# Kernel tuning notes

Measured on AMD Instinct MI355X. Metric: run time of the kernel, lower is better.

Reference implementation:

```python
import jax, jax.numpy as jnp
import numpy as np

TAU = 0.7        # init kwarg tau
BIG_NEG = -1.0e9 # matches torch big_neg
B, R = 8192, 4096


def setup_inputs() -> dict:
    key = jax.random.key(0)
    k1, k2 = jax.random.split(key)
    s = jax.random.normal(k1, (B, R), dtype=jnp.float32)
    mask = jax.random.uniform(k2, (B, R), dtype=jnp.float32)  # compared against 0.5
    return {"s": s, "mask": mask, "k": 8}


def reference(s, mask, k):
    # mask-apply then temperature scale
    z = jnp.where(mask > 0.5, s, jnp.full_like(s, BIG_NEG)) / max(TAU, 1e-6)
    # sparsemax along axis 1: sort descending, cumsum, support-size threshold
    z_sorted = -jnp.sort(-z, axis=1)                       # [B, R] descending
    z_cumsum = jnp.cumsum(z_sorted, axis=1)                # [B, R]
    r = jnp.arange(1, R + 1, dtype=z.dtype)[None, :]       # [1, R] ranks 1..R
    cond = 1.0 + r * z_sorted > z_cumsum                   # [B, R] support indicator
    k_sup = jnp.sum(cond, axis=1, keepdims=True)           # [B, 1] int support size
    tau_star = (jnp.take_along_axis(z_cumsum, k_sup - 1, axis=1) - 1.0) / k_sup.astype(z.dtype)
    p = jnp.maximum(z - tau_star, 0.0)                     # sparsemax probs, sum=1
    # scale by budget k and clip to [0, 1]
    return jnp.minimum(jnp.asarray(float(k), z.dtype) * p, 1.0)
```

## Files before the change

### kernel.cpp

```cpp
#include <hip/hip_runtime.h>


#define R_DIM 4096
#define LANES 64
#define CHUNKS (R_DIM / (LANES * 4))
#define ROWS_PER_BLOCK 4
#define BIG_NEG -1.0e9f
#define INV_TAU (1.0f / 0.7f)

__global__ __launch_bounds__(256, 2)
void gate_sparsemax_k_kernel(const float* __restrict__ s,
                             const float* __restrict__ m,
                             const int*  __restrict__ kptr,
                             float* __restrict__ out,
                             int nrows)
{
    __shared__ float zs[ROWS_PER_BLOCK][R_DIM];

    const int lane = (int)(threadIdx.x & 63u);
    const int wid  = (int)(threadIdx.x >> 6);
    const int row  = blockIdx.x * ROWS_PER_BLOCK + wid;
    if (row >= nrows) return;

    const float kf = (float)(*kptr);

    const size_t base = (size_t)row * R_DIM;
    const float4* sv4 = (const float4*)(s + base);
    const float4* mv4 = (const float4*)(m + base);
    float4*       ov4 = (float4*)(out + base);
    float4*       zr4 = (float4*)(zs[wid]);

    float zmax = -3.4028235e38f;
    #pragma unroll
    for (int c = 0; c < CHUNKS; ++c) {
        const int idx = c * LANES + lane;
        const float4 sv = sv4[idx];
        const float4 mv = mv4[idx];
        float4 zv;
        zv.x = (mv.x > 0.5f ? sv.x : BIG_NEG) * INV_TAU;
        zv.y = (mv.y > 0.5f ? sv.y : BIG_NEG) * INV_TAU;
        zv.z = (mv.z > 0.5f ? sv.z : BIG_NEG) * INV_TAU;
        zv.w = (mv.w > 0.5f ? sv.w : BIG_NEG) * INV_TAU;
        zr4[idx] = zv;
        zmax = fmaxf(zmax, fmaxf(fmaxf(zv.x, zv.y), fmaxf(zv.z, zv.w)));
    }

    #pragma unroll
    for (int off = 32; off >= 1; off >>= 1)
        zmax = fmaxf(zmax, __shfl_xor(zmax, off, 64));

    float tau = zmax - 1.0f;
    for (int it = 0; it < 50; ++it) {
        float ssum = 0.0f;
        float cnt  = 0.0f;
        #pragma unroll
        for (int c = 0; c < CHUNKS; ++c) {
            const float4 zv = zr4[c * LANES + lane];
            if (zv.x > tau) { ssum += zv.x; cnt += 1.0f; }
            if (zv.y > tau) { ssum += zv.y; cnt += 1.0f; }
            if (zv.z > tau) { ssum += zv.z; cnt += 1.0f; }
            if (zv.w > tau) { ssum += zv.w; cnt += 1.0f; }
        }
        #pragma unroll
        for (int off = 32; off >= 1; off >>= 1) {
            ssum += __shfl_xor(ssum, off, 64);
            cnt  += __shfl_xor(cnt,  off, 64);
        }
        const float tnew = (ssum - 1.0f) / cnt;
        if (tnew == tau) break;
        tau = tnew;
    }

    #pragma unroll
    for (int c = 0; c < CHUNKS; ++c) {
        const int idx = c * LANES + lane;
        const float4 zv = zr4[idx];
        float4 ov;
        ov.x = fminf(kf * fmaxf(zv.x - tau, 0.0f), 1.0f);
        ov.y = fminf(kf * fmaxf(zv.y - tau, 0.0f), 1.0f);
        ov.z = fminf(kf * fmaxf(zv.z - tau, 0.0f), 1.0f);
        ov.w = fminf(kf * fmaxf(zv.w - tau, 0.0f), 1.0f);
        ov4[idx] = ov;
    }
}

extern "C" void kernel_launch(void* const* d_in, const int* in_sizes, int n_in,
                              void* d_out, int out_size, void* d_ws, size_t ws_size,
                              hipStream_t stream) {
    const float* s = (const float*)d_in[0];
    const float* m = (const float*)d_in[1];
    const int*   k = (const int*)d_in[2];
    float* out = (float*)d_out;

    const int nrows = in_sizes[0] / R_DIM;
    const int blocks = (nrows + ROWS_PER_BLOCK - 1) / ROWS_PER_BLOCK;

    gate_sparsemax_k_kernel<<<blocks, 256, 0, stream>>>(s, m, k, out, nrows);
}
```

Before: 319.4 us.

## Use one block per row with register-resident values instead of LDS

Each 256-thread block now handles a single row, and every thread keeps its 16 values in registers rather than staging the row in 64KB of shared memory. The change removes the large LDS allocation that limited occupancy and avoids repeated LDS reads on every fixed-point iteration. In exchange, the iteration now needs cross-wave reductions through shared memory with two __syncthreads per iteration. Launch bounds are raised to 6 blocks per CU.

```diff
diff --git a/kernel.cpp b/kernel.cpp
--- a/kernel.cpp
+++ b/kernel.cpp
@@ -2,25 +2,25 @@
 
 
 #define R_DIM 4096
-#define LANES 64
-#define CHUNKS (R_DIM / (LANES * 4))
-#define ROWS_PER_BLOCK 4
+#define BLOCK 256
+#define V4T   4
 #define BIG_NEG -1.0e9f
 #define INV_TAU (1.0f / 0.7f)
 
-__global__ __launch_bounds__(256, 2)
+__global__ __launch_bounds__(BLOCK, 6)
 void gate_sparsemax_k_kernel(const float* __restrict__ s,
                              const float* __restrict__ m,
                              const int*  __restrict__ kptr,
-                             float* __restrict__ out,
-                             int nrows)
+                             float* __restrict__ out)
 {
-    __shared__ float zs[ROWS_PER_BLOCK][R_DIM];
+    __shared__ float red_sum[4];
+    __shared__ float red_cnt[4];
+    __shared__ float red_max[4];
 
-    const int lane = (int)(threadIdx.x & 63u);
-    const int wid  = (int)(threadIdx.x >> 6);
-    const int row  = blockIdx.x * ROWS_PER_BLOCK + wid;
-    if (row >= nrows) return;
+    const int tid  = (int)threadIdx.x;
+    const int lane = tid & 63;
+    const int wid  = tid >> 6;
+    const int row  = (int)blockIdx.x;
 
     const float kf = (float)(*kptr);
 
@@ -28,34 +28,39 @@
     const float4* sv4 = (const float4*)(s + base);
     const float4* mv4 = (const float4*)(m + base);
     float4*       ov4 = (float4*)(out + base);
-    float4*       zr4 = (float4*)(zs[wid]);
 
+    float4 sv[V4T], mv[V4T];
+    #pragma unroll
+    for (int t = 0; t < V4T; ++t) sv[t] = sv4[t * BLOCK + tid];
+    #pragma unroll
+    for (int t = 0; t < V4T; ++t) mv[t] = mv4[t * BLOCK + tid];
+
+    float4 zz[V4T];
     float zmax = -3.4028235e38f;
     #pragma unroll
-    for (int c = 0; c < CHUNKS; ++c) {
-        const int idx = c * LANES + lane;
-        const float4 sv = sv4[idx];
-        const float4 mv = mv4[idx];
+    for (int t = 0; t < V4T; ++t) {
         float4 zv;
-        zv.x = (mv.x > 0.5f ? sv.x : BIG_NEG) * INV_TAU;
-        zv.y = (mv.y > 0.5f ? sv.y : BIG_NEG) * INV_TAU;
-        zv.z = (mv.z > 0.5f ? sv.z : BIG_NEG) * INV_TAU;
-        zv.w = (mv.w > 0.5f ? sv.w : BIG_NEG) * INV_TAU;
-        zr4[idx] = zv;
+        zv.x = (mv[t].x > 0.5f ? sv[t].x : BIG_NEG) * INV_TAU;
+        zv.y = (mv[t].y > 0.5f ? sv[t].y : BIG_NEG) * INV_TAU;
+        zv.z = (mv[t].z > 0.5f ? sv[t].z : BIG_NEG) * INV_TAU;
+        zv.w = (mv[t].w > 0.5f ? sv[t].w : BIG_NEG) * INV_TAU;
+        zz[t] = zv;
         zmax = fmaxf(zmax, fmaxf(fmaxf(zv.x, zv.y), fmaxf(zv.z, zv.w)));
     }
 
     #pragma unroll
     for (int off = 32; off >= 1; off >>= 1)
         zmax = fmaxf(zmax, __shfl_xor(zmax, off, 64));
+    if (lane == 0) red_max[wid] = zmax;
+    __syncthreads();
+    zmax = fmaxf(fmaxf(red_max[0], red_max[1]), fmaxf(red_max[2], red_max[3]));
 
     float tau = zmax - 1.0f;
     for (int it = 0; it < 50; ++it) {
-        float ssum = 0.0f;
-        float cnt  = 0.0f;
+        float ssum = 0.0f, cnt = 0.0f;
         #pragma unroll
-        for (int c = 0; c < CHUNKS; ++c) {
-            const float4 zv = zr4[c * LANES + lane];
+        for (int t = 0; t < V4T; ++t) {
+            const float4 zv = zz[t];
             if (zv.x > tau) { ssum += zv.x; cnt += 1.0f; }
             if (zv.y > tau) { ssum += zv.y; cnt += 1.0f; }
             if (zv.z > tau) { ssum += zv.z; cnt += 1.0f; }
@@ -66,21 +71,25 @@
             ssum += __shfl_xor(ssum, off, 64);
             cnt  += __shfl_xor(cnt,  off, 64);
         }
-        const float tnew = (ssum - 1.0f) / cnt;
+        __syncthreads();
+        if (lane == 0) { red_sum[wid] = ssum; red_cnt[wid] = cnt; }
+        __syncthreads();
+        const float S = ((red_sum[0] + red_sum[1]) + (red_sum[2] + red_sum[3]));
+        const float C = ((red_cnt[0] + red_cnt[1]) + (red_cnt[2] + red_cnt[3]));
+        const float tnew = (S - 1.0f) / C;
         if (tnew == tau) break;
         tau = tnew;
     }
 
     #pragma unroll
-    for (int c = 0; c < CHUNKS; ++c) {
-        const int idx = c * LANES + lane;
-        const float4 zv = zr4[idx];
+    for (int t = 0; t < V4T; ++t) {
+        const float4 zv = zz[t];
         float4 ov;
         ov.x = fminf(kf * fmaxf(zv.x - tau, 0.0f), 1.0f);
         ov.y = fminf(kf * fmaxf(zv.y - tau, 0.0f), 1.0f);
         ov.z = fminf(kf * fmaxf(zv.z - tau, 0.0f), 1.0f);
         ov.w = fminf(kf * fmaxf(zv.w - tau, 0.0f), 1.0f);
-        ov4[idx] = ov;
+        ov4[t * BLOCK + tid] = ov;
     }
 }
 
@@ -93,7 +102,5 @@
     float* out = (float*)d_out;
 
     const int nrows = in_sizes[0] / R_DIM;
-    const int blocks = (nrows + ROWS_PER_BLOCK - 1) / ROWS_PER_BLOCK;
-
-    gate_sparsemax_k_kernel<<<blocks, 256, 0, stream>>>(s, m, k, out, nrows);
+    gate_sparsemax_k_kernel<<<nrows, BLOCK, 0, stream>>>(s, m, k, out);
 }
```

Result: faster. 312.4 us (-2.2%).
